# Kernel optimization log

Measured on AMD Instinct MI355X. Metric: run time of the kernel, lower is better.

Reference implementation:

```python
import jax, jax.numpy as jnp
import numpy as np

TAU = 0.2  # temperature

def setup_inputs() -> dict:
    key = jax.random.key(0)
    k1, k2, k3 = jax.random.split(key, 3)
    query = jax.random.normal(k1, (8192, 128), dtype=jnp.float32)
    pos = jax.random.normal(k2, (8192, 128), dtype=jnp.float32)
    neg = jax.random.normal(k3, (16384, 128), dtype=jnp.float32)
    return {"query": query, "pos": pos, "neg": neg}

def reference(query, pos, neg):
    # scores: [N, M] = query @ neg^T / tau
    scores = jnp.einsum('nd,md->nm', query, neg) / TAU
    # positive logits: [N]
    pos_logit = jnp.sum(query * pos, axis=-1) / TAU
    # loss = mean_n( logsumexp_m(scores) - pos_logit )
    lse = jax.scipy.special.logsumexp(scores, axis=-1)
    return jnp.mean(lse - pos_logit)
```

## Files before the change

kernel.cpp:

```cpp
#include <hip/hip_runtime.h>
#include <cstdint>

#define NQ    8192
#define NNEG  16384
#define DIM   128
#define SPLIT 16
#define CHUNK (NNEG / SPLIT)
#define K_SCALE 7.2134752044448169f
#define LN2     0.69314718055994531f

typedef __attribute__((ext_vector_type(8))) __bf16 bf16x8;
typedef __attribute__((ext_vector_type(4))) float  f32x4;

__device__ inline void async_load16(const void* g, void* l) {
    __builtin_amdgcn_global_load_lds(
        (const __attribute__((address_space(1))) void*)g,
        (__attribute__((address_space(3))) void*)l, 16, 0, 0);
}

__device__ inline unsigned short f2bf(float x) {
    uint32_t u = __float_as_uint(x);
    u += 0x7fffu + ((u >> 16) & 1u);
    return (unsigned short)(u >> 16);
}

__device__ inline float waveReduceSum(float v) {
#pragma unroll
    for (int m = 32; m >= 1; m >>= 1) v += __shfl_xor(v, m, 64);
    return v;
}

__global__ __launch_bounds__(256) void iw_prep(
    const float* __restrict__ q, const float* __restrict__ p,
    const float* __restrict__ neg,
    unsigned short* __restrict__ qb, unsigned short* __restrict__ nb,
    float* __restrict__ out)
{
    const int tid = threadIdx.x;
    const int i = blockIdx.x * 256 + tid;
    constexpr int QG = NQ * DIM / 4;
    if (i < QG) {
        float4 v = ((const float4*)q)[i];
        ushort4 o;
        o.x = f2bf(v.x * K_SCALE); o.y = f2bf(v.y * K_SCALE);
        o.z = f2bf(v.z * K_SCALE); o.w = f2bf(v.w * K_SCALE);
        ((ushort4*)qb)[i] = o;
        float4 pv = ((const float4*)p)[i];
        float acc = fmaf(v.x, pv.x, fmaf(v.y, pv.y, fmaf(v.z, pv.z, v.w * pv.w)));
        acc = waveReduceSum(acc);
        __shared__ float red[4];
        if ((tid & 63) == 0) red[tid >> 6] = acc;
        __syncthreads();
        if (tid == 0) {
            float s = red[0] + red[1] + red[2] + red[3];
            atomicAdd(out, s * (-1.0f / (0.2f * (float)NQ)));
        }
    } else {
        int j = i - QG;
        float4 v = ((const float4*)neg)[j];
        ushort4 o;
        o.x = f2bf(v.x); o.y = f2bf(v.y); o.z = f2bf(v.z); o.w = f2bf(v.w);
        ((ushort4*)nb)[j] = o;
    }
}

__global__ __launch_bounds__(256, 4) void iw_main(
    const unsigned short* __restrict__ qb, const unsigned short* __restrict__ nb,
    float2* __restrict__ partial)
{
    constexpr int BM = 128, BN = 64, NIT = CHUNK / BN;
    __shared__ alignas(16) unsigned short n_lds[2 * BN * DIM];

    const int tid  = threadIdx.x;
    const int lane = tid & 63;
    const int w    = tid >> 6;
    const int quad = lane >> 4;
    const int c0   = lane & 15;

    const int row0   = blockIdx.x * BM;
    const int nbase0 = blockIdx.y * CHUNK;

    bf16x8 afrag[2][4];
#pragma unroll
    for (int rs = 0; rs < 2; ++rs)
#pragma unroll
        for (int ks = 0; ks < 4; ++ks) {
            const int qrow = row0 + w * 32 + rs * 16 + c0;
            afrag[rs][ks] = *reinterpret_cast<const bf16x8*>(
                qb + (size_t)qrow * DIM + ks * 32 + quad * 8);
        }

    int nro[4], ndst[4];
#pragma unroll
    for (int pp = 0; pp < 4; ++pp) {
        int t   = w * 4 + pp;
        int idx = t * 64 + lane;
        int r   = idx >> 4;
        int kb  = (idx & 15) ^ (r & 15);
        nro[pp]  = r * DIM + kb * 8;
        ndst[pp] = t * 512;
    }
#pragma unroll
    for (int pp = 0; pp < 4; ++pp)
        async_load16(nb + (size_t)nbase0 * DIM + nro[pp], n_lds + ndst[pp]);
    __syncthreads();

    float m_s[2][4], l_s[2][4];
#pragma unroll
    for (int rs = 0; rs < 2; ++rs)
#pragma unroll
        for (int i = 0; i < 4; ++i) { m_s[rs][i] = -1e30f; l_s[rs][i] = 0.f; }

    const f32x4 zero4 = {0.f, 0.f, 0.f, 0.f};

    for (int it = 0; it < NIT; ++it) {
        const int buf  = (it & 1) * (BN * DIM);
        if (it + 1 < NIT) {
            const unsigned short* src = nb + (size_t)(nbase0 + (it + 1) * BN) * DIM;
            const int nbuf = ((it + 1) & 1) * (BN * DIM);
#pragma unroll
            for (int pp = 0; pp < 4; ++pp)
                async_load16(src + nro[pp], n_lds + nbuf + ndst[pp]);
        }

        f32x4 acc[2][4];
#pragma unroll
        for (int rs = 0; rs < 2; ++rs)
#pragma unroll
            for (int ns = 0; ns < 4; ++ns) acc[rs][ns] = zero4;

#pragma unroll
        for (int ns = 0; ns < 4; ++ns) {
#pragma unroll
            for (int ks = 0; ks < 4; ++ks) {
                int blk = (ns * 16 + c0) * 16 + ((ks * 4 + quad) ^ c0);
                bf16x8 b = *reinterpret_cast<const bf16x8*>(n_lds + buf + blk * 8);
                acc[0][ns] = __builtin_amdgcn_mfma_f32_16x16x32_bf16(afrag[0][ks], b, acc[0][ns], 0, 0, 0);
                acc[1][ns] = __builtin_amdgcn_mfma_f32_16x16x32_bf16(afrag[1][ks], b, acc[1][ns], 0, 0, 0);
            }
        }

#pragma unroll
        for (int rs = 0; rs < 2; ++rs) {
#pragma unroll
            for (int i = 0; i < 4; ++i) {
                float y0 = acc[rs][0][i], y1 = acc[rs][1][i];
                float y2 = acc[rs][2][i], y3 = acc[rs][3][i];
                float mx = fmaxf(fmaxf(y0, y1), fmaxf(y2, y3));
                float m0 = m_s[rs][i];
                float nm = fmaxf(m0, mx);
                float t  = __builtin_amdgcn_exp2f(y0 - nm) + __builtin_amdgcn_exp2f(y1 - nm)
                         + __builtin_amdgcn_exp2f(y2 - nm) + __builtin_amdgcn_exp2f(y3 - nm);
                l_s[rs][i] = l_s[rs][i] * __builtin_amdgcn_exp2f(m0 - nm) + t;
                m_s[rs][i] = nm;
            }
        }
        __syncthreads();
    }

#pragma unroll
    for (int rs = 0; rs < 2; ++rs) {
#pragma unroll
        for (int i = 0; i < 4; ++i) {
            float m = m_s[rs][i], l = l_s[rs][i];
#pragma unroll
            for (int s = 1; s < 16; s <<= 1) {
                float om = __shfl_xor(m, s, 64);
                float ol = __shfl_xor(l, s, 64);
                float nm = fmaxf(m, om);
                l = l * __builtin_amdgcn_exp2f(m - nm) + ol * __builtin_amdgcn_exp2f(om - nm);
                m = nm;
            }
            if (c0 == 0) {
                int grow = row0 + w * 32 + rs * 16 + quad * 4 + i;
                partial[(size_t)blockIdx.y * NQ + grow] = make_float2(m, l);
            }
        }
    }
}

__global__ __launch_bounds__(256) void iw_merge(
    const float2* __restrict__ partial, float* __restrict__ out)
{
    const int tid = threadIdx.x;
    const int row = blockIdx.x * 256 + tid;
    float M = -1e30f, L = 0.f;
#pragma unroll
    for (int c = 0; c < SPLIT; ++c) {
        float2 p = partial[(size_t)c * NQ + row];
        float nm = fmaxf(M, p.x);
        L = L * __builtin_amdgcn_exp2f(M - nm) + p.y * __builtin_amdgcn_exp2f(p.x - nm);
        M = nm;
    }
    float lse = LN2 * (M + __log2f(L));
    float v = lse * (1.0f / (float)NQ);
    v = waveReduceSum(v);
    __shared__ float red[4];
    if ((tid & 63) == 0) red[tid >> 6] = v;
    __syncthreads();
    if (tid == 0) atomicAdd(out, red[0] + red[1] + red[2] + red[3]);
}

extern "C" void kernel_launch(void* const* d_in, const int* in_sizes, int n_in,
                              void* d_out, int out_size, void* d_ws, size_t ws_size,
                              hipStream_t stream) {
    const float* q   = (const float*)d_in[0];
    const float* pos = (const float*)d_in[1];
    const float* neg = (const float*)d_in[2];
    float* out = (float*)d_out;

    unsigned short* qb = (unsigned short*)d_ws;
    unsigned short* nb = qb + (size_t)NQ * DIM;
    float2* partial    = (float2*)(nb + (size_t)NNEG * DIM);

    hipMemsetAsync(out, 0, sizeof(float), stream);
    iw_prep <<<3072, 256, 0, stream>>>(q, pos, neg, qb, nb, out);
    iw_main <<<dim3(NQ / 128, SPLIT), 256, 0, stream>>>(qb, nb, partial);
    iw_merge<<<32,   256, 0, stream>>>(partial, out);
}
```

Before: 133.0 us.

## Switch score GEMM from bf16 to fp8 MFMA with 16x16x128 scaled instructions

Query and negative embeddings are now quantized to FP8 instead of bf16 in the prep kernel. The main kernel uses the MI355X scaled f8f6f4 MFMA (16x16x128), so each output tile needs one MFMA per row-slice instead of four. LDS footprint and global traffic for negatives are halved, with a new swizzle for 32-byte groups. The trade-off is lower precision on the logits (scaled by 1/tau·log2e before quantization), which may hurt accuracy of the logsumexp loss.

```diff
diff --git a/kernel.cpp b/kernel.cpp
--- a/kernel.cpp
+++ b/kernel.cpp
@@ -9,8 +9,10 @@
 #define K_SCALE 7.2134752044448169f
 #define LN2     0.69314718055994531f
 
-typedef __attribute__((ext_vector_type(8))) __bf16 bf16x8;
-typedef __attribute__((ext_vector_type(4))) float  f32x4;
+typedef __attribute__((ext_vector_type(8))) int   i32x8;
+typedef __attribute__((ext_vector_type(4))) float f32x4;
+
+union U8 { i32x8 v; int4 h[2]; };
 
 __device__ inline void async_load16(const void* g, void* l) {
     __builtin_amdgcn_global_load_lds(
@@ -18,12 +20,6 @@
         (__attribute__((address_space(3))) void*)l, 16, 0, 0);
 }
 
-__device__ inline unsigned short f2bf(float x) {
-    uint32_t u = __float_as_uint(x);
-    u += 0x7fffu + ((u >> 16) & 1u);
-    return (unsigned short)(u >> 16);
-}
-
 __device__ inline float waveReduceSum(float v) {
 #pragma unroll
     for (int m = 32; m >= 1; m >>= 1) v += __shfl_xor(v, m, 64);
@@ -33,20 +29,24 @@
 __global__ __launch_bounds__(256) void iw_prep(
     const float* __restrict__ q, const float* __restrict__ p,
     const float* __restrict__ neg,
-    unsigned short* __restrict__ qb, unsigned short* __restrict__ nb,
+    unsigned char* __restrict__ qb8, unsigned char* __restrict__ nb8,
     float* __restrict__ out)
 {
     const int tid = threadIdx.x;
-    const int i = blockIdx.x * 256 + tid;
-    constexpr int QG = NQ * DIM / 4;
-    if (i < QG) {
-        float4 v = ((const float4*)q)[i];
-        ushort4 o;
-        o.x = f2bf(v.x * K_SCALE); o.y = f2bf(v.y * K_SCALE);
-        o.z = f2bf(v.z * K_SCALE); o.w = f2bf(v.w * K_SCALE);
-        ((ushort4*)qb)[i] = o;
-        float4 pv = ((const float4*)p)[i];
-        float acc = fmaf(v.x, pv.x, fmaf(v.y, pv.y, fmaf(v.z, pv.z, v.w * pv.w)));
+    const int t = blockIdx.x * 256 + tid;
+    constexpr int QT = NQ * DIM / 8;
+    if (t < QT) {
+        const float4* q4 = (const float4*)q;
+        float4 v0 = q4[t * 2], v1 = q4[t * 2 + 1];
+        int w0 = __builtin_amdgcn_cvt_pk_fp8_f32(v0.x * K_SCALE, v0.y * K_SCALE, 0, false);
+        w0     = __builtin_amdgcn_cvt_pk_fp8_f32(v0.z * K_SCALE, v0.w * K_SCALE, w0, true);
+        int w1 = __builtin_amdgcn_cvt_pk_fp8_f32(v1.x * K_SCALE, v1.y * K_SCALE, 0, false);
+        w1     = __builtin_amdgcn_cvt_pk_fp8_f32(v1.z * K_SCALE, v1.w * K_SCALE, w1, true);
+        ((int2*)qb8)[t] = make_int2(w0, w1);
+        const float4* p4 = (const float4*)p;
+        float4 p0 = p4[t * 2], p1 = p4[t * 2 + 1];
+        float acc = fmaf(v0.x, p0.x, fmaf(v0.y, p0.y, fmaf(v0.z, p0.z, v0.w * p0.w)));
+        acc = fmaf(v1.x, p1.x, fmaf(v1.y, p1.y, fmaf(v1.z, p1.z, fmaf(v1.w, p1.w, acc))));
         acc = waveReduceSum(acc);
         __shared__ float red[4];
         if ((tid & 63) == 0) red[tid >> 6] = acc;
@@ -56,20 +56,23 @@
             atomicAdd(out, s * (-1.0f / (0.2f * (float)NQ)));
         }
     } else {
-        int j = i - QG;
-        float4 v = ((const float4*)neg)[j];
-        ushort4 o;
-        o.x = f2bf(v.x); o.y = f2bf(v.y); o.z = f2bf(v.z); o.w = f2bf(v.w);
-        ((ushort4*)nb)[j] = o;
+        int j = t - QT;
+        const float4* n4 = (const float4*)neg;
+        float4 v0 = n4[j * 2], v1 = n4[j * 2 + 1];
+        int w0 = __builtin_amdgcn_cvt_pk_fp8_f32(v0.x, v0.y, 0, false);
+        w0     = __builtin_amdgcn_cvt_pk_fp8_f32(v0.z, v0.w, w0, true);
+        int w1 = __builtin_amdgcn_cvt_pk_fp8_f32(v1.x, v1.y, 0, false);
+        w1     = __builtin_amdgcn_cvt_pk_fp8_f32(v1.z, v1.w, w1, true);
+        ((int2*)nb8)[j] = make_int2(w0, w1);
     }
 }
 
 __global__ __launch_bounds__(256, 4) void iw_main(
-    const unsigned short* __restrict__ qb, const unsigned short* __restrict__ nb,
+    const unsigned char* __restrict__ qb8, const unsigned char* __restrict__ nb8,
     float2* __restrict__ partial)
 {
     constexpr int BM = 128, BN = 64, NIT = CHUNK / BN;
-    __shared__ alignas(16) unsigned short n_lds[2 * BN * DIM];
+    __shared__ alignas(16) unsigned char n_lds[2 * BN * DIM];
 
     const int tid  = threadIdx.x;
     const int lane = tid & 63;
@@ -80,64 +83,61 @@
     const int row0   = blockIdx.x * BM;
     const int nbase0 = blockIdx.y * CHUNK;
 
-    bf16x8 afrag[2][4];
+    U8 afrag[2];
+#pragma unroll
+    for (int rs = 0; rs < 2; ++rs) {
+        const int qrow = row0 + w * 32 + rs * 16 + c0;
+        const int4* pa = reinterpret_cast<const int4*>(qb8 + (size_t)qrow * DIM + quad * 32);
+        afrag[rs].h[0] = pa[0];
+        afrag[rs].h[1] = pa[1];
+    }
+
+    int srcoff[2], dstoff[2];
+#pragma unroll
+    for (int j = 0; j < 2; ++j) {
+        int L  = (w * 2 + j) * 64 + lane;
+        int h  = L & 1, G = L >> 1;
+        int r  = G >> 2;
+        int kb = (G & 3) ^ (r & 3);
+        srcoff[j] = r * DIM + kb * 32 + h * 16;
+        dstoff[j] = (w * 2 + j) * 1024;
+    }
+#pragma unroll
+    for (int j = 0; j < 2; ++j)
+        async_load16(nb8 + (size_t)nbase0 * DIM + srcoff[j], n_lds + dstoff[j]);
+    __syncthreads();
+
+    float m_s[2][4], l_s[2][4];
 #pragma unroll
     for (int rs = 0; rs < 2; ++rs)
 #pragma unroll
-        for (int ks = 0; ks < 4; ++ks) {
-            const int qrow = row0 + w * 32 + rs * 16 + c0;
-            afrag[rs][ks] = *reinterpret_cast<const bf16x8*>(
-                qb + (size_t)qrow * DIM + ks * 32 + quad * 8);
-        }
-
-    int nro[4], ndst[4];
-#pragma unroll
-    for (int pp = 0; pp < 4; ++pp) {
-        int t   = w * 4 + pp;
-        int idx = t * 64 + lane;
-        int r   = idx >> 4;
-        int kb  = (idx & 15) ^ (r & 15);
-        nro[pp]  = r * DIM + kb * 8;
-        ndst[pp] = t * 512;
-    }
-#pragma unroll
-    for (int pp = 0; pp < 4; ++pp)
-        async_load16(nb + (size_t)nbase0 * DIM + nro[pp], n_lds + ndst[pp]);
-    __syncthreads();
-
-    float m_s[2][4], l_s[2][4];
-#pragma unroll
-    for (int rs = 0; rs < 2; ++rs)
-#pragma unroll
         for (int i = 0; i < 4; ++i) { m_s[rs][i] = -1e30f; l_s[rs][i] = 0.f; }
 
     const f32x4 zero4 = {0.f, 0.f, 0.f, 0.f};
 
     for (int it = 0; it < NIT; ++it) {
-        const int buf  = (it & 1) * (BN * DIM);
+        const int buf = (it & 1) * (BN * DIM);
         if (it + 1 < NIT) {
-            const unsigned short* src = nb + (size_t)(nbase0 + (it + 1) * BN) * DIM;
+            const unsigned char* src = nb8 + (size_t)(nbase0 + (it + 1) * BN) * DIM;
             const int nbuf = ((it + 1) & 1) * (BN * DIM);
 #pragma unroll
-            for (int pp = 0; pp < 4; ++pp)
-                async_load16(src + nro[pp], n_lds + nbuf + ndst[pp]);
+            for (int j = 0; j < 2; ++j)
+                async_load16(src + srcoff[j], n_lds + nbuf + dstoff[j]);
         }
 
         f32x4 acc[2][4];
 #pragma unroll
-        for (int rs = 0; rs < 2; ++rs)
-#pragma unroll
-            for (int ns = 0; ns < 4; ++ns) acc[rs][ns] = zero4;
-
-#pragma unroll
         for (int ns = 0; ns < 4; ++ns) {
-#pragma unroll
-            for (int ks = 0; ks < 4; ++ks) {
-                int blk = (ns * 16 + c0) * 16 + ((ks * 4 + quad) ^ c0);
-                bf16x8 b = *reinterpret_cast<const bf16x8*>(n_lds + buf + blk * 8);
-                acc[0][ns] = __builtin_amdgcn_mfma_f32_16x16x32_bf16(afrag[0][ks], b, acc[0][ns], 0, 0, 0);
-                acc[1][ns] = __builtin_amdgcn_mfma_f32_16x16x32_bf16(afrag[1][ks], b, acc[1][ns], 0, 0, 0);
-            }
+            int c  = ns * 16 + c0;
+            int g0 = (c << 2) + (quad ^ (c & 3));
+            const int4* pb = reinterpret_cast<const int4*>(n_lds + buf + g0 * 32);
+            U8 b;
+            b.h[0] = pb[0];
+            b.h[1] = pb[1];
+            acc[0][ns] = __builtin_amdgcn_mfma_scale_f32_16x16x128_f8f6f4(
+                afrag[0].v, b.v, zero4, 0, 0, 0, 127, 0, 127);
+            acc[1][ns] = __builtin_amdgcn_mfma_scale_f32_16x16x128_f8f6f4(
+                afrag[1].v, b.v, zero4, 0, 0, 0, 127, 0, 127);
         }
 
 #pragma unroll
@@ -209,12 +209,12 @@
     const float* neg = (const float*)d_in[2];
     float* out = (float*)d_out;
 
-    unsigned short* qb = (unsigned short*)d_ws;
-    unsigned short* nb = qb + (size_t)NQ * DIM;
-    float2* partial    = (float2*)(nb + (size_t)NNEG * DIM);
+    unsigned char* qb8 = (unsigned char*)d_ws;
+    unsigned char* nb8 = qb8 + (size_t)NQ * DIM;
+    float2* partial    = (float2*)(nb8 + (size_t)NNEG * DIM);
 
     hipMemsetAsync(out, 0, sizeof(float), stream);
-    iw_prep <<<3072, 256, 0, stream>>>(q, pos, neg, qb, nb, out);
-    iw_main <<<dim3(NQ / 128, SPLIT), 256, 0, stream>>>(qb, nb, partial);
+    iw_prep <<<1536, 256, 0, stream>>>(q, pos, neg, qb8, nb8, out);
+    iw_main <<<dim3(NQ / 128, SPLIT), 256, 0, stream>>>(qb8, nb8, partial);
     iw_merge<<<32,   256, 0, stream>>>(partial, out);
 }
```

New measurement: 112.6 us. 1.18x faster.
